# Kernel optimization log

Hardware: AMD Instinct MI355X
Metric: run time of the kernel (lower is better)

Reference implementation:

```python
import jax, jax.numpy as jnp
import numpy as np

EXP, MAN = 8, 23  # exponent/mantissa bits of the simulated float format


def float_quantize(x, exp=EXP, man=MAN):
    """Round-to-nearest-even quantization to a float format with `exp` exponent
    bits and `man` mantissa bits (faithful to mptorch float_quantize 'nearest').
    With exp=8, man=23 this is an exact identity on fp32 inputs."""
    emax = 2 ** (exp - 1) - 1          # max unbiased exponent
    emin = 1 - emax                     # min normal exponent (clamping here yields subnormal grid)
    ax = jnp.abs(x)
    e = jnp.clip(jnp.floor(jnp.log2(jnp.where(ax > 0, ax, 1.0))), emin, emax)
    # scale mantissa into [1,2), round to `man` fractional bits (ties-to-even via jnp.round)
    m = jnp.round(x * jnp.exp2(-e) * (2.0 ** man)) * (2.0 ** -man)
    q = m * jnp.exp2(e)
    maxval = (2.0 - 2.0 ** -man) * (2.0 ** emax)
    q = jnp.clip(q, -maxval, maxval)
    return jnp.where(ax == 0, x, q).astype(x.dtype)


def setup_inputs() -> dict:
    key = jax.random.key(0)
    k1, k2, k3 = jax.random.split(key, 3)
    M, IN, OUT = 8192, 1024, 4096
    x = jax.random.normal(k1, (M, IN), dtype=jnp.float32)
    # kaiming-uniform-ish scale for weight, 1/sqrt(fan_in) for bias
    bound_w = float(np.sqrt(1.0 / IN))
    weight = jax.random.uniform(k2, (OUT, IN), dtype=jnp.float32, minval=-bound_w, maxval=bound_w)
    bias = jax.random.uniform(k3, (OUT,), dtype=jnp.float32, minval=-bound_w, maxval=bound_w)
    return {"x": x, "weight": weight, "bias": bias}


def reference(x, weight, bias):
    # QLinearFunction.forward: quantize weight, quant_gemm, add quantized bias, quantize output.
    # quant_gemm with (man=23, exp=8) simulates fp32 multiply-accumulate, i.e. a plain
    # fp32 GEMM; we express it as matmul followed by output quantization.
    qweight = float_quantize(weight)                 # [OUT, IN]
    out = jnp.matmul(x, qweight.T)                   # [M, OUT], fp32 accumulate
    out = out + float_quantize(bias)[None, :]
    return float_quantize(out)
```

## Files before the change

### kernel.cpp

```cpp
#include <hip/hip_runtime.h>
#include <stdint.h>

#define MM 8192
#define KK 1024
#define NN 4096
#define NT 32

typedef float f32x16 __attribute__((ext_vector_type(16)));
typedef __bf16 bf16x8 __attribute__((ext_vector_type(8)));
typedef unsigned short u16x8 __attribute__((ext_vector_type(8)));

static __device__ __forceinline__ unsigned short f2bf(float f) {
    unsigned int u = __builtin_bit_cast(unsigned int, f);
    u += 0x7fffu + ((u >> 16) & 1u);
    return (unsigned short)(u >> 16);
}
static __device__ __forceinline__ float bf2f(unsigned short s) {
    unsigned int u = ((unsigned int)s) << 16;
    return __builtin_bit_cast(float, u);
}

__global__ __launch_bounds__(256) void pack_a(const float* __restrict__ x,
        unsigned short* __restrict__ Ah, unsigned short* __restrict__ Al) {
    int i = blockIdx.x * 256 + threadIdx.x;
    int lane = i & 63, fb = (i >> 6) & 15, kt = (i >> 10) & 31, bm = i >> 15;
    int row = bm * 256 + (fb >> 1) * 32 + (lane & 31);
    int k   = kt * 32 + (fb & 1) * 16 + (lane >> 5) * 8;
    const float4* s = (const float4*)(x + (size_t)row * KK + k);
    float4 a = s[0], b = s[1];
    float v[8] = {a.x, a.y, a.z, a.w, b.x, b.y, b.z, b.w};
    u16x8 h, l;
#pragma unroll
    for (int j = 0; j < 8; ++j) {
        unsigned short hb = f2bf(v[j]);
        h[j] = hb;
        l[j] = f2bf(v[j] - bf2f(hb));
    }
    *(u16x8*)(Ah + (size_t)i * 8) = h;
    *(u16x8*)(Al + (size_t)i * 8) = l;
}

__global__ __launch_bounds__(256) void pack_b(const float* __restrict__ w,
        unsigned short* __restrict__ Bpk) {
    int i = blockIdx.x * 256 + threadIdx.x;
    int lane = i & 63, fb = (i >> 6) & 7, kt = (i >> 9) & 31, bn = i >> 14;
    int col = bn * 128 + (fb >> 1) * 32 + (lane & 31);
    int k   = kt * 32 + (fb & 1) * 16 + (lane >> 5) * 8;
    const float4* s = (const float4*)(w + (size_t)col * KK + k);
    float4 a = s[0], b = s[1];
    float v[8] = {a.x, a.y, a.z, a.w, b.x, b.y, b.z, b.w};
    u16x8 h, l;
#pragma unroll
    for (int j = 0; j < 8; ++j) {
        unsigned short hb = f2bf(v[j]);
        h[j] = hb;
        l[j] = f2bf(v[j] - bf2f(hb));
    }
    size_t tb = ((size_t)bn * 32 + kt) * 8192;
    *(u16x8*)(Bpk + tb + fb * 512 + lane * 8) = h;
    *(u16x8*)(Bpk + tb + 4096 + fb * 512 + lane * 8) = l;
}

static __device__ __forceinline__ void gl16(const unsigned short* g, unsigned short* l) {
    __builtin_amdgcn_global_load_lds(
        (__attribute__((address_space(1))) void*)(void*)g,
        (__attribute__((address_space(3))) void*)(void*)l, 16, 0, 0);
}
static __device__ __forceinline__ void mf(f32x16& d, bf16x8 a, bf16x8 b) {
    d = __builtin_amdgcn_mfma_f32_32x32x16_bf16(a, b, d, 0, 0, 0);
}

__global__ __launch_bounds__(256, 2) void qlinear_mfma(
        const unsigned short* __restrict__ Ah, const unsigned short* __restrict__ Al,
        const unsigned short* __restrict__ Bpk,
        const float* __restrict__ bias, float* __restrict__ out) {
    __shared__ __attribute__((aligned(16))) unsigned short sB[2 * 8192];

    int bid = blockIdx.x;
    int xc = bid & 7, s = bid >> 3;
    int bm = (xc & 3) * 8 + (s & 7);
    int bn = (xc >> 2) * 16 + (s >> 3);

    const int tid = threadIdx.x;
    const int lane = tid & 63, wid = tid >> 6;
    const int wrb = (wid >> 1) * 4;
    const int wcb = (wid & 1) * 2;

    const size_t aoff = (size_t)bm * 262144 + (size_t)wrb * 1024 + lane * 8;
    const size_t bsrc = (size_t)bn * 262144 + tid * 8;
    const unsigned boff = wcb * 1024 + lane * 8;

    f32x16 acc[4][2];
#pragma unroll
    for (int mi = 0; mi < 4; ++mi)
#pragma unroll
        for (int ni = 0; ni < 2; ++ni)
#pragma unroll
            for (int r = 0; r < 16; ++r) acc[mi][ni][r] = 0.f;

    bf16x8 A0h[4], A0l[4], A1h[4], A1l[4];

#define LDA(H, L, T, KS) do { _Pragma("unroll") \
    for (int mi = 0; mi < 4; ++mi) { \
        H[mi] = *(const bf16x8*)(Ah + aoff + (size_t)(T) * 8192 + mi * 1024 + (KS) * 512); \
        L[mi] = *(const bf16x8*)(Al + aoff + (size_t)(T) * 8192 + mi * 1024 + (KS) * 512); \
    } } while (0)
#define STB(T, NB) do { _Pragma("unroll") \
    for (int j = 0; j < 4; ++j) \
        gl16(Bpk + bsrc + (size_t)(T) * 8192 + j * 2048, \
             sB + (NB) * 8192 + j * 2048 + tid * 8); } while (0)

    LDA(A0h, A0l, 0, 0);
    LDA(A1h, A1l, 0, 1);
    STB(0, 0);
    __syncthreads();

    for (int t = 0; t < NT; ++t) {
        const int cur = t & 1, nb = cur ^ 1;
        const unsigned short* sb = sB + cur * 8192;

        bf16x8 B0h[2], B0l[2], B1h[2], B1l[2];
#pragma unroll
        for (int ni = 0; ni < 2; ++ni) {
            B0h[ni] = *(const bf16x8*)(sb + boff + ni * 1024);
            B0l[ni] = *(const bf16x8*)(sb + 4096 + boff + ni * 1024);
        }
        if (t + 1 < NT) STB(t + 1, nb);

        __builtin_amdgcn_s_setprio(1);
#pragma unroll
        for (int mi = 0; mi < 4; ++mi)
#pragma unroll
            for (int ni = 0; ni < 2; ++ni) mf(acc[mi][ni], A0h[mi], B0h[ni]);
#pragma unroll
        for (int mi = 0; mi < 4; ++mi)
#pragma unroll
            for (int ni = 0; ni < 2; ++ni) mf(acc[mi][ni], A0l[mi], B0h[ni]);
#pragma unroll
        for (int mi = 0; mi < 4; ++mi)
#pragma unroll
            for (int ni = 0; ni < 2; ++ni) mf(acc[mi][ni], A0h[mi], B0l[ni]);
        __builtin_amdgcn_s_setprio(0);
        __builtin_amdgcn_sched_barrier(0);
        if (t + 1 < NT) LDA(A0h, A0l, t + 1, 0);

#pragma unroll
        for (int ni = 0; ni < 2; ++ni) {
            B1h[ni] = *(const bf16x8*)(sb + boff + ni * 1024 + 512);
            B1l[ni] = *(const bf16x8*)(sb + 4096 + boff + ni * 1024 + 512);
        }
        __builtin_amdgcn_s_setprio(1);
#pragma unroll
        for (int mi = 0; mi < 4; ++mi)
#pragma unroll
            for (int ni = 0; ni < 2; ++ni) mf(acc[mi][ni], A1h[mi], B1h[ni]);
#pragma unroll
        for (int mi = 0; mi < 4; ++mi)
#pragma unroll
            for (int ni = 0; ni < 2; ++ni) mf(acc[mi][ni], A1l[mi], B1h[ni]);
#pragma unroll
        for (int mi = 0; mi < 4; ++mi)
#pragma unroll
            for (int ni = 0; ni < 2; ++ni) mf(acc[mi][ni], A1h[mi], B1l[ni]);
        __builtin_amdgcn_s_setprio(0);
        __builtin_amdgcn_sched_barrier(0);
        if (t + 1 < NT) LDA(A1h, A1l, t + 1, 1);

        __syncthreads();
    }
#undef LDA
#undef STB

    const int row0 = bm * 256 + (wid >> 1) * 128 + 4 * (lane >> 5);
    const int col0 = bn * 128 + (wid & 1) * 64 + (lane & 31);
    float bv[2] = {bias[col0], bias[col0 + 32]};
#pragma unroll
    for (int mi = 0; mi < 4; ++mi)
#pragma unroll
        for (int ni = 0; ni < 2; ++ni)
#pragma unroll
            for (int r = 0; r < 16; ++r) {
                int rr = row0 + mi * 32 + (r & 3) + 8 * (r >> 2);
                out[(size_t)rr * NN + col0 + ni * 32] = acc[mi][ni][r] + bv[ni];
            }
}

__global__ __launch_bounds__(256) void qlinear_naive(const float* __restrict__ x,
                                                     const float* __restrict__ w,
                                                     const float* __restrict__ bias,
                                                     float* __restrict__ out) {
    int n = blockIdx.x * 64 + (threadIdx.x & 63);
    int m = blockIdx.y * 4 + (threadIdx.x >> 6);
    const float4* xr = (const float4*)(x + (size_t)m * KK);
    const float4* wr = (const float4*)(w + (size_t)n * KK);
    float s = 0.f;
    for (int k = 0; k < KK / 4; ++k) {
        float4 a = xr[k], b = wr[k];
        s += a.x * b.x + a.y * b.y + a.z * b.z + a.w * b.w;
    }
    out[(size_t)m * NN + n] = s + bias[n];
}

extern "C" void kernel_launch(void* const* d_in, const int* in_sizes, int n_in,
                              void* d_out, int out_size, void* d_ws, size_t ws_size,
                              hipStream_t stream) {
    (void)in_sizes; (void)n_in; (void)out_size;
    const float* x = (const float*)d_in[0];
    const float* w = (const float*)d_in[1];
    const float* bias = (const float*)d_in[2];
    float* out = (float*)d_out;

    const size_t xcnt = (size_t)MM * KK;
    const size_t wcnt = (size_t)NN * KK;
    const size_t need = (2 * xcnt + 2 * wcnt) * sizeof(unsigned short);

    if (ws_size >= need) {
        unsigned short* Ahp = (unsigned short*)d_ws;
        unsigned short* Alp = Ahp + xcnt;
        unsigned short* Bp  = Alp + xcnt;
        pack_a<<<(int)(xcnt / 8 / 256), 256, 0, stream>>>(x, Ahp, Alp);
        pack_b<<<(int)(wcnt / 8 / 256), 256, 0, stream>>>(w, Bp);
        qlinear_mfma<<<1024, 256, 0, stream>>>(Ahp, Alp, Bp, bias, out);
    } else {
        dim3 grid(NN / 64, MM / 4);
        qlinear_naive<<<grid, 256, 0, stream>>>(x, w, bias, out);
    }
}
```

Baseline: 344.4 us.

## Restructure split-bf16 GEMM into 256x256 tiles with LDS-staged A and B

The main GEMM kernel is rebuilt around 512-thread blocks computing 256x256 output tiles. Both A and B hi/lo planes are now staged through double-buffered LDS using global_load_lds, where before A was read straight into registers from global memory. The kernel switches from 32x32x16 to 16x16x32 bf16 MFMA and uses barrier/waitcnt-fenced phases with setprio to overlap prefetch with compute. The pack kernels are changed to write matching interleaved layouts. The aim is more data reuse per tile and less global traffic, in exchange for 128 KB of LDS, heavier register use and a more fragile hand-written synchronisation scheme.

```diff
diff --git a/kernel.cpp b/kernel.cpp
--- a/kernel.cpp
+++ b/kernel.cpp
@@ -4,9 +4,8 @@
 #define MM 8192
 #define KK 1024
 #define NN 4096
-#define NT 32
-
-typedef float f32x16 __attribute__((ext_vector_type(16)));
+
+typedef float f32x4 __attribute__((ext_vector_type(4)));
 typedef __bf16 bf16x8 __attribute__((ext_vector_type(8)));
 typedef unsigned short u16x8 __attribute__((ext_vector_type(8)));
 
@@ -21,11 +20,11 @@
 }
 
 __global__ __launch_bounds__(256) void pack_a(const float* __restrict__ x,
-        unsigned short* __restrict__ Ah, unsigned short* __restrict__ Al) {
+                                              unsigned short* __restrict__ Apk) {
     int i = blockIdx.x * 256 + threadIdx.x;
-    int lane = i & 63, fb = (i >> 6) & 15, kt = (i >> 10) & 31, bm = i >> 15;
-    int row = bm * 256 + (fb >> 1) * 32 + (lane & 31);
-    int k   = kt * 32 + (fb & 1) * 16 + (lane >> 5) * 8;
+    int lane = i & 63, g = (i >> 6) & 15, kt = (i >> 10) & 31, bm = i >> 15;
+    int row = bm * 256 + g * 16 + (lane & 15);
+    int k   = kt * 32 + (lane >> 4) * 8;
     const float4* s = (const float4*)(x + (size_t)row * KK + k);
     float4 a = s[0], b = s[1];
     float v[8] = {a.x, a.y, a.z, a.w, b.x, b.y, b.z, b.w};
@@ -36,16 +35,18 @@
         h[j] = hb;
         l[j] = f2bf(v[j] - bf2f(hb));
     }
-    *(u16x8*)(Ah + (size_t)i * 8) = h;
-    *(u16x8*)(Al + (size_t)i * 8) = l;
+    size_t tb = (size_t)(bm * 32 + kt) * 16384;
+    size_t fo = (size_t)g * 512 + lane * 8;
+    *(u16x8*)(Apk + tb + fo) = h;
+    *(u16x8*)(Apk + tb + 8192 + fo) = l;
 }
 
 __global__ __launch_bounds__(256) void pack_b(const float* __restrict__ w,
-        unsigned short* __restrict__ Bpk) {
+                                              unsigned short* __restrict__ Bpk) {
     int i = blockIdx.x * 256 + threadIdx.x;
-    int lane = i & 63, fb = (i >> 6) & 7, kt = (i >> 9) & 31, bn = i >> 14;
-    int col = bn * 128 + (fb >> 1) * 32 + (lane & 31);
-    int k   = kt * 32 + (fb & 1) * 16 + (lane >> 5) * 8;
+    int lane = i & 63, g = (i >> 6) & 15, kt = (i >> 10) & 31, bn = i >> 15;
+    int col = bn * 256 + g * 16 + (lane & 15);
+    int k   = kt * 32 + (lane >> 4) * 8;
     const float4* s = (const float4*)(w + (size_t)col * KK + k);
     float4 a = s[0], b = s[1];
     float v[8] = {a.x, a.y, a.z, a.w, b.x, b.y, b.z, b.w};
@@ -56,133 +57,144 @@
         h[j] = hb;
         l[j] = f2bf(v[j] - bf2f(hb));
     }
-    size_t tb = ((size_t)bn * 32 + kt) * 8192;
-    *(u16x8*)(Bpk + tb + fb * 512 + lane * 8) = h;
-    *(u16x8*)(Bpk + tb + 4096 + fb * 512 + lane * 8) = l;
-}
-
+    size_t tb = (size_t)(bn * 32 + kt) * 16384;
+    size_t fo = (size_t)g * 512 + lane * 8;
+    *(u16x8*)(Bpk + tb + fo) = h;
+    *(u16x8*)(Bpk + tb + 8192 + fo) = l;
+}
+
+static __device__ __forceinline__ bf16x8 ldsr(unsigned addr) {
+    bf16x8 r;
+    asm volatile("ds_read_b128 %0, %1" : "=v"(r) : "v"(addr));
+    return r;
+}
 static __device__ __forceinline__ void gl16(const unsigned short* g, unsigned short* l) {
     __builtin_amdgcn_global_load_lds(
         (__attribute__((address_space(1))) void*)(void*)g,
         (__attribute__((address_space(3))) void*)(void*)l, 16, 0, 0);
 }
-static __device__ __forceinline__ void mf(f32x16& d, bf16x8 a, bf16x8 b) {
-    d = __builtin_amdgcn_mfma_f32_32x32x16_bf16(a, b, d, 0, 0, 0);
-}
-
-__global__ __launch_bounds__(256, 2) void qlinear_mfma(
-        const unsigned short* __restrict__ Ah, const unsigned short* __restrict__ Al,
-        const unsigned short* __restrict__ Bpk,
+
+__global__ __launch_bounds__(512, 2) void qlinear_mfma(
+        const unsigned short* __restrict__ Apk, const unsigned short* __restrict__ Bpk,
         const float* __restrict__ bias, float* __restrict__ out) {
-    __shared__ __attribute__((aligned(16))) unsigned short sB[2 * 8192];
+    __shared__ __attribute__((aligned(16))) unsigned short S[2][4][8192];
 
     int bid = blockIdx.x;
-    int xc = bid & 7, s = bid >> 3;
-    int bm = (xc & 3) * 8 + (s & 7);
-    int bn = (xc >> 2) * 16 + (s >> 3);
+    int xcd = bid & 7, sq = bid >> 3;
+    int bm = xcd * 4 + (sq & 3);
+    int bn = sq >> 2;
 
     const int tid = threadIdx.x;
     const int lane = tid & 63, wid = tid >> 6;
-    const int wrb = (wid >> 1) * 4;
-    const int wcb = (wid & 1) * 2;
-
-    const size_t aoff = (size_t)bm * 262144 + (size_t)wrb * 1024 + lane * 8;
-    const size_t bsrc = (size_t)bn * 262144 + tid * 8;
-    const unsigned boff = wcb * 1024 + lane * 8;
-
-    f32x16 acc[4][2];
-#pragma unroll
-    for (int mi = 0; mi < 4; ++mi)
-#pragma unroll
-        for (int ni = 0; ni < 2; ++ni)
-#pragma unroll
-            for (int r = 0; r < 16; ++r) acc[mi][ni][r] = 0.f;
-
-    bf16x8 A0h[4], A0l[4], A1h[4], A1l[4];
-
-#define LDA(H, L, T, KS) do { _Pragma("unroll") \
-    for (int mi = 0; mi < 4; ++mi) { \
-        H[mi] = *(const bf16x8*)(Ah + aoff + (size_t)(T) * 8192 + mi * 1024 + (KS) * 512); \
-        L[mi] = *(const bf16x8*)(Al + aoff + (size_t)(T) * 8192 + mi * 1024 + (KS) * 512); \
+    const int wr2 = wid >> 2;
+    const int wc2 = wid & 3;
+    const int lr = lane & 15, lg = lane >> 4;
+
+    const unsigned lb = (unsigned)(uintptr_t)(__attribute__((address_space(3))) void*)&S[0][0][0];
+    const unsigned fragA = (unsigned)((wr2 * 8) * 1024 + lane * 16);
+    const unsigned fragB = (unsigned)((wc2 * 4) * 1024 + lane * 16);
+
+    const size_t abase = (size_t)bm * 524288;
+    const size_t bbase = (size_t)bn * 524288;
+
+#define STP(SRCE, BUF, PLN) do {                                   \
+        gl16((SRCE) + tid * 8,        &S[BUF][PLN][tid * 8]);      \
+        gl16((SRCE) + 4096 + tid * 8, &S[BUF][PLN][4096 + tid * 8]); } while (0)
+
+#define OPEN()                                                     \
+    __builtin_amdgcn_s_barrier();                                  \
+    asm volatile("s_waitcnt lgkmcnt(0)" ::: "memory");             \
+    __builtin_amdgcn_sched_barrier(0);                             \
+    __builtin_amdgcn_s_setprio(1)
+#define CLOSE()                                                    \
+    __builtin_amdgcn_s_setprio(0);                                 \
+    __builtin_amdgcn_sched_barrier(0);                             \
+    __builtin_amdgcn_s_barrier()
+#define CLOSEW(N)                                                  \
+    __builtin_amdgcn_s_setprio(0);                                 \
+    __builtin_amdgcn_sched_barrier(0);                             \
+    asm volatile("s_waitcnt vmcnt(" #N ")" ::: "memory");          \
+    __builtin_amdgcn_s_barrier()
+#define MF16(AARR, M0, BARR) do { _Pragma("unroll")                \
+    for (int mi = 0; mi < 4; ++mi) { _Pragma("unroll")             \
+        for (int ni = 0; ni < 4; ++ni)                             \
+            acc[(M0) + mi][ni] = __builtin_amdgcn_mfma_f32_16x16x32_bf16( \
+                AARR[(M0) + mi], BARR[ni], acc[(M0) + mi][ni], 0, 0, 0);  \
     } } while (0)
-#define STB(T, NB) do { _Pragma("unroll") \
-    for (int j = 0; j < 4; ++j) \
-        gl16(Bpk + bsrc + (size_t)(T) * 8192 + j * 2048, \
-             sB + (NB) * 8192 + j * 2048 + tid * 8); } while (0)
-
-    LDA(A0h, A0l, 0, 0);
-    LDA(A1h, A1l, 0, 1);
-    STB(0, 0);
-    __syncthreads();
-
-    for (int t = 0; t < NT; ++t) {
-        const int cur = t & 1, nb = cur ^ 1;
-        const unsigned short* sb = sB + cur * 8192;
-
-        bf16x8 B0h[2], B0l[2], B1h[2], B1l[2];
-#pragma unroll
-        for (int ni = 0; ni < 2; ++ni) {
-            B0h[ni] = *(const bf16x8*)(sb + boff + ni * 1024);
-            B0l[ni] = *(const bf16x8*)(sb + 4096 + boff + ni * 1024);
+
+    f32x4 acc[8][4];
+#pragma unroll
+    for (int mi = 0; mi < 8; ++mi)
+#pragma unroll
+        for (int ni = 0; ni < 4; ++ni) acc[mi][ni] = (f32x4){0.f, 0.f, 0.f, 0.f};
+
+    bf16x8 Ahf[8], Alf[8], Bhf[4], Blf[4];
+
+    STP(Apk + abase, 0, 0);
+    STP(Bpk + bbase, 0, 2);
+    STP(Apk + abase + 8192, 0, 1);
+    STP(Bpk + bbase + 8192, 0, 3);
+    asm volatile("s_waitcnt vmcnt(4)" ::: "memory");
+    __builtin_amdgcn_s_barrier();
+
+    for (int ct = 0; ct < 32; ++ct) {
+        const int cur = ct & 1, nb = cur ^ 1;
+        const unsigned cb = lb + (unsigned)cur * 65536u;
+        const unsigned short* nA = Apk + abase + (size_t)(ct + 1) * 16384;
+        const unsigned short* nB = Bpk + bbase + (size_t)(ct + 1) * 16384;
+        const bool pf = (ct < 31);
+
+#pragma unroll
+        for (int mi = 0; mi < 4; ++mi) Ahf[mi] = ldsr(cb + fragA + mi * 1024u);
+#pragma unroll
+        for (int ni = 0; ni < 4; ++ni) Bhf[ni] = ldsr(cb + 32768u + fragB + ni * 1024u);
+        if (pf) STP(nA, nb, 0);
+        OPEN(); MF16(Ahf, 0, Bhf); CLOSE();
+
+#pragma unroll
+        for (int mi = 4; mi < 8; ++mi) Ahf[mi] = ldsr(cb + fragA + mi * 1024u);
+        if (pf) STP(nB, nb, 2);
+        OPEN(); MF16(Ahf, 4, Bhf);
+        if (pf) { CLOSEW(6); } else { CLOSEW(2); }
+
+#pragma unroll
+        for (int mi = 0; mi < 4; ++mi) Alf[mi] = ldsr(cb + 16384u + fragA + mi * 1024u);
+        if (pf) STP(nA + 8192, nb, 1);
+        OPEN(); MF16(Alf, 0, Bhf); CLOSE();
+
+#pragma unroll
+        for (int mi = 4; mi < 8; ++mi) Alf[mi] = ldsr(cb + 16384u + fragA + mi * 1024u);
+        if (pf) STP(nB + 8192, nb, 3);
+        OPEN(); MF16(Alf, 4, Bhf);
+        if (pf) { CLOSEW(8); } else { CLOSEW(0); }
+
+#pragma unroll
+        for (int ni = 0; ni < 4; ++ni) Blf[ni] = ldsr(cb + 49152u + fragB + ni * 1024u);
+        OPEN(); MF16(Ahf, 0, Blf); CLOSE();
+
+        OPEN(); MF16(Ahf, 4, Blf);
+        if (pf) { CLOSEW(4); } else { CLOSE(); }
+    }
+#undef STP
+#undef OPEN
+#undef CLOSE
+#undef CLOSEW
+#undef MF16
+
+    const int row0 = bm * 256 + wr2 * 128 + lg * 4;
+    const int col0 = bn * 256 + wc2 * 64 + lr;
+    float bv[4];
+#pragma unroll
+    for (int ni = 0; ni < 4; ++ni) bv[ni] = bias[col0 + ni * 16];
+#pragma unroll
+    for (int mi = 0; mi < 8; ++mi)
+#pragma unroll
+        for (int ni = 0; ni < 4; ++ni) {
+            float* o = out + (size_t)(row0 + mi * 16) * NN + col0 + ni * 16;
+#pragma unroll
+            for (int r = 0; r < 4; ++r)
+                o[(size_t)r * NN] = acc[mi][ni][r] + bv[ni];
         }
-        if (t + 1 < NT) STB(t + 1, nb);
-
-        __builtin_amdgcn_s_setprio(1);
-#pragma unroll
-        for (int mi = 0; mi < 4; ++mi)
-#pragma unroll
-            for (int ni = 0; ni < 2; ++ni) mf(acc[mi][ni], A0h[mi], B0h[ni]);
-#pragma unroll
-        for (int mi = 0; mi < 4; ++mi)
-#pragma unroll
-            for (int ni = 0; ni < 2; ++ni) mf(acc[mi][ni], A0l[mi], B0h[ni]);
-#pragma unroll
-        for (int mi = 0; mi < 4; ++mi)
-#pragma unroll
-            for (int ni = 0; ni < 2; ++ni) mf(acc[mi][ni], A0h[mi], B0l[ni]);
-        __builtin_amdgcn_s_setprio(0);
-        __builtin_amdgcn_sched_barrier(0);
-        if (t + 1 < NT) LDA(A0h, A0l, t + 1, 0);
-
-#pragma unroll
-        for (int ni = 0; ni < 2; ++ni) {
-            B1h[ni] = *(const bf16x8*)(sb + boff + ni * 1024 + 512);
-            B1l[ni] = *(const bf16x8*)(sb + 4096 + boff + ni * 1024 + 512);
-        }
-        __builtin_amdgcn_s_setprio(1);
-#pragma unroll
-        for (int mi = 0; mi < 4; ++mi)
-#pragma unroll
-            for (int ni = 0; ni < 2; ++ni) mf(acc[mi][ni], A1h[mi], B1h[ni]);
-#pragma unroll
-        for (int mi = 0; mi < 4; ++mi)
-#pragma unroll
-            for (int ni = 0; ni < 2; ++ni) mf(acc[mi][ni], A1l[mi], B1h[ni]);
-#pragma unroll
-        for (int mi = 0; mi < 4; ++mi)
-#pragma unroll
-            for (int ni = 0; ni < 2; ++ni) mf(acc[mi][ni], A1h[mi], B1l[ni]);
-        __builtin_amdgcn_s_setprio(0);
-        __builtin_amdgcn_sched_barrier(0);
-        if (t + 1 < NT) LDA(A1h, A1l, t + 1, 1);
-
-        __syncthreads();
-    }
-#undef LDA
-#undef STB
-
-    const int row0 = bm * 256 + (wid >> 1) * 128 + 4 * (lane >> 5);
-    const int col0 = bn * 128 + (wid & 1) * 64 + (lane & 31);
-    float bv[2] = {bias[col0], bias[col0 + 32]};
-#pragma unroll
-    for (int mi = 0; mi < 4; ++mi)
-#pragma unroll
-        for (int ni = 0; ni < 2; ++ni)
-#pragma unroll
-            for (int r = 0; r < 16; ++r) {
-                int rr = row0 + mi * 32 + (r & 3) + 8 * (r >> 2);
-                out[(size_t)rr * NN + col0 + ni * 32] = acc[mi][ni][r] + bv[ni];
-            }
 }
 
 __global__ __launch_bounds__(256) void qlinear_naive(const float* __restrict__ x,
@@ -215,12 +227,11 @@
     const size_t need = (2 * xcnt + 2 * wcnt) * sizeof(unsigned short);
 
     if (ws_size >= need) {
-        unsigned short* Ahp = (unsigned short*)d_ws;
-        unsigned short* Alp = Ahp + xcnt;
-        unsigned short* Bp  = Alp + xcnt;
-        pack_a<<<(int)(xcnt / 8 / 256), 256, 0, stream>>>(x, Ahp, Alp);
-        pack_b<<<(int)(wcnt / 8 / 256), 256, 0, stream>>>(w, Bp);
-        qlinear_mfma<<<1024, 256, 0, stream>>>(Ahp, Alp, Bp, bias, out);
+        unsigned short* Apk = (unsigned short*)d_ws;
+        unsigned short* Bpk = Apk + 2 * xcnt;
+        pack_a<<<(int)(xcnt / 8 / 256), 256, 0, stream>>>(x, Apk);
+        pack_b<<<(int)(wcnt / 8 / 256), 256, 0, stream>>>(w, Bpk);
+        qlinear_mfma<<<512, 512, 0, stream>>>(Apk, Bpk, bias, out);
     } else {
         dim3 grid(NN / 64, MM / 4);
         qlinear_naive<<<grid, 256, 0, stream>>>(x, w, bias, out);
```

Result: faster. 325.4 us (-5.5%).
